# Optimization experiments

Hardware: AMD Instinct MI355X
Metric: run time of the kernel (lower is better)

Reference implementation:

```python
import jax, jax.numpy as jnp
import numpy as np

N, E = 50000, 400000
IN_CH, HID, HEADS, EDGE_DIM = 128, 64, 4, 3
NEG_SLOPE = 0.2


def gatv2_conv(x, src, dst, edge_attr, Wl, Wr, We, att, bias):
    # x: [N, F_in]; Wl/Wr: [H*C, F_in]; We: [H*C, edge_dim]; att: [H, C]; bias: [C]
    H, C = att.shape
    n = x.shape[0]
    xl = (x @ Wl.T).reshape(n, H, C)   # source-side transform (lin_l)
    xr = (x @ Wr.T).reshape(n, H, C)   # target-side transform (lin_r)
    e = (edge_attr @ We.T).reshape(-1, H, C)
    z = jax.nn.leaky_relu(xl[src] + xr[dst] + e, NEG_SLOPE)  # [E,H,C]
    alpha = jnp.einsum('ehc,hc->eh', z, att)                 # [E,H]
    # segment softmax over incoming edges per destination node
    amax = jax.ops.segment_max(alpha, dst, num_segments=n)
    alpha = jnp.exp(alpha - amax[dst])
    denom = jax.ops.segment_sum(alpha, dst, num_segments=n)
    alpha = alpha / (denom[dst] + 1e-16)
    msg = xl[src] * alpha[:, :, None]                        # [E,H,C]
    out = jax.ops.segment_sum(msg, dst, num_segments=n)      # [N,H,C]
    return out.mean(axis=1) + bias                           # concat=False -> head mean


def setup_inputs() -> dict:
    key = jax.random.key(0)
    ks = jax.random.split(key, 16)
    s = 0.1
    return {
        'x': jax.random.normal(ks[0], (N, IN_CH), jnp.float32),
        'edge_index': jax.random.randint(ks[1], (2, E), 0, N, jnp.int32),
        'edge_attr': jax.random.normal(ks[2], (E, EDGE_DIM), jnp.float32),
        'Wl1': jax.random.normal(ks[3], (HEADS * HID, IN_CH), jnp.float32) * s,
        'Wr1': jax.random.normal(ks[4], (HEADS * HID, IN_CH), jnp.float32) * s,
        'We1': jax.random.normal(ks[5], (HEADS * HID, EDGE_DIM), jnp.float32) * s,
        'att1': jax.random.normal(ks[6], (HEADS, HID), jnp.float32) * s,
        'b1': jnp.zeros((HID,), jnp.float32),
        'Wl2': jax.random.normal(ks[7], (HEADS * HID, HID), jnp.float32) * s,
        'Wr2': jax.random.normal(ks[8], (HEADS * HID, HID), jnp.float32) * s,
        'We2': jax.random.normal(ks[9], (HEADS * HID, EDGE_DIM), jnp.float32) * s,
        'att2': jax.random.normal(ks[10], (HEADS, HID), jnp.float32) * s,
        'b2': jnp.zeros((HID,), jnp.float32),
        'prelu_w': jnp.full((HID,), 0.25, jnp.float32),
    }


def reference(x, edge_index, edge_attr, Wl1, Wr1, We1, att1, b1, Wl2, Wr2, We2, att2, b2, prelu_w):
    src, dst = edge_index[0], edge_index[1]
    h = gatv2_conv(x, src, dst, edge_attr, Wl1, Wr1, We1, att1, b1)
    h = gatv2_conv(h, src, dst, edge_attr, Wl2, Wr2, We2, att2, b2)
    return jnp.where(h >= 0, h, prelu_w * h)  # PReLU, per-channel weight
```

## Files before the change

### kernel.cpp

```cpp
#include <hip/hip_runtime.h>
#include <hip/hip_bf16.h>

#define HC 256

typedef __attribute__((ext_vector_type(8))) short bf16x8;
typedef __attribute__((ext_vector_type(4))) float f32x4;
typedef __attribute__((ext_vector_type(2))) float f32x2;

__device__ __forceinline__ void gl_lds16(const void* g, void* l) {
  __builtin_amdgcn_global_load_lds(
      (const __attribute__((address_space(1))) unsigned int*)g,
      (__attribute__((address_space(3))) unsigned int*)l, 16, 0, 0);
}

__device__ __forceinline__ void cast_w_one(const float* Wl, const float* Wr,
                                           ushort* WT, int F, int idx) {
  int col = idx / F, f = idx - col * F;
  float v = (col < 256) ? Wl[col * F + f] : Wr[(col - 256) * F + f];
  __hip_bfloat16 h = __float2bfloat16(v);
  WT[(size_t)col * F + f] = *(ushort*)&h;
}

__global__ void k_weights_hist(const float* __restrict__ Wl1, const float* __restrict__ Wr1,
                               ushort* __restrict__ WT1, const float* __restrict__ Wl2,
                               const float* __restrict__ Wr2, ushort* __restrict__ WT2,
                               const int* __restrict__ ei, int* __restrict__ deg, int E_) {
  int idx = blockIdx.x * blockDim.x + threadIdx.x;
  const int t1 = 512 * 128, t2 = 512 * 64;
  if (idx < t1) {
    cast_w_one(Wl1, Wr1, WT1, 128, idx);
  } else if (idx < t1 + t2) {
    cast_w_one(Wl2, Wr2, WT2, 64, idx - t1);
  } else {
    int e = idx - t1 - t2;
    if (e < E_) atomicAdd(&deg[ei[E_ + e]], 1);
  }
}

template <int F>
__global__ __launch_bounds__(256) void gemm_mfma(const ushort* __restrict__ A,
                                                 const ushort* __restrict__ WT,
                                                 ushort* __restrict__ xlb,
                                                 ushort* __restrict__ xrb, int n_nodes) {
  constexpr int NSTEP = F / 64;
  constexpr int SM = (2 * NSTEP * 8192 > 17408) ? 2 * NSTEP * 8192 : 17408;
  __shared__ __align__(16) ushort smem[SM];
  const int tid = threadIdx.x;
  const int wv = tid >> 6, lane = tid & 63;
  const int m16 = lane & 15, quad = lane >> 4;
  const int col0 = blockIdx.x * 128;
  const int row0 = blockIdx.y * 128;
  const int wm = (wv >> 1) * 64, wn = (wv & 1) * 64;

  f32x4 acc[4][4];
#pragma unroll
  for (int i = 0; i < 4; ++i)
#pragma unroll
    for (int j = 0; j < 4; ++j) acc[i][j] = (f32x4){0.f, 0.f, 0.f, 0.f};

  auto load_step = [&](int s) {
    ushort* As = smem + s * 16384;
    ushort* Bs = As + 8192;
    const int khat = s * 64;
#pragma unroll
    for (int t = 0; t < 4; ++t) {
      const int sl16 = tid + 256 * t;
      const int row = sl16 >> 3, sl = sl16 & 7;
      const int gch = sl ^ (row & 7);
      const int grow = row0 + row;
      if (grow < n_nodes)
        gl_lds16(A + (size_t)grow * F + khat + gch * 8, As + sl16 * 8);
      gl_lds16(WT + (size_t)(col0 + row) * F + khat + gch * 8, Bs + sl16 * 8);
    }
  };

  auto mfma_step = [&](int s) {
    ushort* As = smem + s * 16384;
    ushort* Bs = As + 8192;
#pragma unroll
    for (int kh = 0; kh < 2; ++kh) {
      bf16x8 af[4], bf[4];
#pragma unroll
      for (int i = 0; i < 4; ++i) {
        const int row = wm + i * 16 + m16;
        const int slot = (kh * 4 + quad) ^ (row & 7);
        af[i] = *(bf16x8*)&As[row * 64 + slot * 8];
      }
#pragma unroll
      for (int j = 0; j < 4; ++j) {
        const int col = wn + j * 16 + m16;
        const int slot = (kh * 4 + quad) ^ (col & 7);
        bf[j] = *(bf16x8*)&Bs[col * 64 + slot * 8];
      }
#pragma unroll
      for (int i = 0; i < 4; ++i)
#pragma unroll
        for (int j = 0; j < 4; ++j)
          acc[i][j] =
              __builtin_amdgcn_mfma_f32_16x16x32_bf16(af[i], bf[j], acc[i][j], 0, 0, 0);
    }
  };

  load_step(0);
  __syncthreads();
  if (NSTEP > 1) load_step(1);
  mfma_step(0);
  if (NSTEP > 1) {
    __syncthreads();
    mfma_step(1);
  }

  __syncthreads();
  ushort* Ct = smem;
#pragma unroll
  for (int i = 0; i < 4; ++i) {
#pragma unroll
    for (int r = 0; r < 4; ++r) {
      const int row = wm + i * 16 + quad * 4 + r;
#pragma unroll
      for (int j = 0; j < 4; ++j) {
        __hip_bfloat16 h = __float2bfloat16(acc[i][j][r]);
        Ct[row * 136 + wn + j * 16 + m16] = *(ushort*)&h;
      }
    }
  }
  __syncthreads();
  const bool is_xl = (col0 < 256);
  ushort* dst = is_xl ? xlb : xrb;
  const int cb = is_xl ? col0 : (col0 - 256);
  const int chunk = tid & 15;
#pragma unroll
  for (int it = 0; it < 8; ++it) {
    const int row = (tid >> 4) + 16 * it;
    const int grow = row0 + row;
    int4 v = *(int4*)&Ct[row * 136 + chunk * 8];
    if (grow < n_nodes)
      *(int4*)(dst + (size_t)grow * 256 + cb + chunk * 8) = v;
  }
}

__global__ void k_scan_local(const int* __restrict__ deg, int* __restrict__ rowstart,
                             int* __restrict__ partial, int n) {
  __shared__ int a[256], b[256];
  const int t = threadIdx.x;
  const int i = blockIdx.x * 256 + t;
  const int v = (i < n) ? deg[i] : 0;
  a[t] = v;
  __syncthreads();
  int* cur = a;
  int* nxt = b;
  for (int off = 1; off < 256; off <<= 1) {
    int x = cur[t];
    if (t >= off) x += cur[t - off];
    nxt[t] = x;
    __syncthreads();
    int* tmp = cur; cur = nxt; nxt = tmp;
  }
  const int incl = cur[t];
  if (i < n) rowstart[i] = incl - v;
  if (t == 255) partial[blockIdx.x] = incl;
}

__global__ void k_scan_final(const int* __restrict__ partial, int nblk,
                             int* __restrict__ rowstart, int* __restrict__ cursor,
                             float4* __restrict__ sea, int n, int E_) {
  __shared__ int a[256], b[256];
  const int t = threadIdx.x;
  const int v = (t < nblk) ? partial[t] : 0;
  a[t] = v;
  __syncthreads();
  int* cur = a;
  int* nxt = b;
  for (int off = 1; off < 256; off <<= 1) {
    int x = cur[t];
    if (t >= off) x += cur[t - off];
    nxt[t] = x;
    __syncthreads();
    int* tmp = cur; cur = nxt; nxt = tmp;
  }
  const int boff = (blockIdx.x > 0) ? cur[blockIdx.x - 1] : 0;
  const int i = blockIdx.x * 256 + t;
  if (i < n) {
    int vv = rowstart[i] + boff;
    rowstart[i] = vv;
    cursor[i] = vv;
  }
  if (i == 0) rowstart[n] = E_;
  if (blockIdx.x == 0 && t < 8) sea[E_ + t] = make_float4(0.f, 0.f, 0.f, 0.f);
}

__global__ void k_prep(const float* __restrict__ x, ushort* __restrict__ A,
                       const int* __restrict__ ei, const float* __restrict__ ea,
                       int* __restrict__ cursor, float4* __restrict__ sea,
                       int n, int E_) {
  const int nx8 = n * 16;
  int idx = blockIdx.x * blockDim.x + threadIdx.x;
  if (idx < nx8) {
    const float4* xp = (const float4*)x + (size_t)idx * 2;
    float4 v0 = xp[0], v1 = xp[1];
    float vv[8] = {v0.x, v0.y, v0.z, v0.w, v1.x, v1.y, v1.z, v1.w};
    __align__(16) ushort hb[8];
#pragma unroll
    for (int j = 0; j < 8; ++j) {
      __hip_bfloat16 h = __float2bfloat16(vv[j]);
      hb[j] = *(ushort*)&h;
    }
    *(int4*)(A + (size_t)idx * 8) = *(int4*)hb;
  } else {
    int e = idx - nx8;
    if (e < E_) {
      int dst = ei[E_ + e];
      int pos = atomicAdd(&cursor[dst], 1);
      sea[pos] = make_float4(ea[e * 3], ea[e * 3 + 1], ea[e * 3 + 2],
                             __int_as_float(ei[e]));
    }
  }
}

__device__ __forceinline__ float dpp_ror_add(float p) {
  p += __int_as_float(__builtin_amdgcn_update_dpp(
      0, __float_as_int(p), 0x128, 0xF, 0xF, true));
  p += __int_as_float(__builtin_amdgcn_update_dpp(
      0, __float_as_int(p), 0x124, 0xF, 0xF, true));
  p += __int_as_float(__builtin_amdgcn_update_dpp(
      0, __float_as_int(p), 0x122, 0xF, 0xF, true));
  p += __int_as_float(__builtin_amdgcn_update_dpp(
      0, __float_as_int(p), 0x121, 0xF, 0xF, true));
  return p;
}

__device__ __forceinline__ void edge_step(
    const ushort4& lu, const float4& eav, const f32x2* we0, const f32x2* we1,
    const f32x2* we2, const f32x2* at6, const f32x2* at4, const f32x2* xrl,
    f32x2& num01, f32x2& num23, float& den) {
  f32x2 lav0, lav1;
  lav0.x = __uint_as_float((unsigned)lu.x << 16);
  lav0.y = __uint_as_float((unsigned)lu.y << 16);
  lav1.x = __uint_as_float((unsigned)lu.z << 16);
  lav1.y = __uint_as_float((unsigned)lu.w << 16);
  f32x2 pv = {0.f, 0.f};
#pragma unroll
  for (int j = 0; j < 2; ++j) {
    f32x2 la = (j == 0) ? lav0 : lav1;
    f32x2 t = xrl[j] + we0[j] * eav.x;
    t = t + we1[j] * eav.y;
    t = t + we2[j] * eav.z;
    f32x2 s = t + la;
    f32x2 sa = {fabsf(s.x), fabsf(s.y)};
    pv = pv + at6[j] * s;
    pv = pv + at4[j] * sa;
  }
  float p = pv.x + pv.y;
  p = dpp_ror_add(p);
  const float w = exp2f(p);
  den += w;
  num01 = num01 + (f32x2){w, w} * lav0;
  num23 = num23 + (f32x2){w, w} * lav1;
}

template <int MODE>
__global__ __launch_bounds__(64) void fused_attn(
    const ushort* __restrict__ xlb, const ushort* __restrict__ xrb,
    const int* __restrict__ rowstart, const float4* __restrict__ sea,
    const float* __restrict__ We, const float* __restrict__ att,
    const float* __restrict__ bias, const float* __restrict__ pw,
    float* __restrict__ out, ushort* __restrict__ outs, int n, int chunk) {
  const int lane = threadIdx.x;
  const int d0 = blockIdx.x * chunk;
  if (d0 >= n) return;
  const int d1 = min(d0 + chunk, n);

  f32x2 we0[2], we1[2], we2[2], at6[2], at4[2];
  const float L2E = 1.4426950408889634f;
#pragma unroll
  for (int j = 0; j < 4; ++j) {
    int r = 4 * lane + j;
    ((float*)we0)[j] = We[r * 3 + 0];
    ((float*)we1)[j] = We[r * 3 + 1];
    ((float*)we2)[j] = We[r * 3 + 2];
    float a = att[r];
    ((float*)at6)[j] = a * (0.6f * L2E);
    ((float*)at4)[j] = a * (0.4f * L2E);
  }
  const float4 bias4 = ((const float4*)bias)[lane & 15];
  float4 pw4 = {0.f, 0.f, 0.f, 0.f};
  if (MODE == 1) pw4 = ((const float4*)pw)[lane & 15];
  const ushort4* xlb4 = (const ushort4*)xlb;

  for (int d = d0; d < d1; ++d) {
    const ushort4 xu = ((const ushort4*)xrb)[(unsigned)(d * 64) + lane];
    f32x2 xrl[2];
    xrl[0].x = __uint_as_float((unsigned)xu.x << 16);
    xrl[0].y = __uint_as_float((unsigned)xu.y << 16);
    xrl[1].x = __uint_as_float((unsigned)xu.z << 16);
    xrl[1].y = __uint_as_float((unsigned)xu.w << 16);

    int pos = rowstart[d];
    const int end = rowstart[d + 1];
    f32x2 num01 = {0.f, 0.f}, num23 = {0.f, 0.f};
    float den = 0.f;

    if (pos < end) {
      float4 e0 = sea[pos], e1 = sea[pos + 1], e2 = sea[pos + 2], e3 = sea[pos + 3];
      ushort4 g0 = xlb4[(unsigned)(__float_as_int(e0.w) * 64) + lane];
      ushort4 g1 = xlb4[(unsigned)(__float_as_int(e1.w) * 64) + lane];
      ushort4 g2 = xlb4[(unsigned)(__float_as_int(e2.w) * 64) + lane];
      ushort4 g3 = xlb4[(unsigned)(__float_as_int(e3.w) * 64) + lane];

      while (pos + 4 <= end) {
        ushort4 h0 = g0, h1 = g1, h2 = g2, h3 = g3;
        float4 f0 = e0, f1 = e1, f2 = e2, f3 = e3;
        if (pos + 4 < end) {
          f0 = sea[pos + 4];
          f1 = sea[pos + 5];
          f2 = sea[pos + 6];
          f3 = sea[pos + 7];
          h0 = xlb4[(unsigned)(__float_as_int(f0.w) * 64) + lane];
          h1 = xlb4[(unsigned)(__float_as_int(f1.w) * 64) + lane];
          h2 = xlb4[(unsigned)(__float_as_int(f2.w) * 64) + lane];
          h3 = xlb4[(unsigned)(__float_as_int(f3.w) * 64) + lane];
        }
        edge_step(g0, e0, we0, we1, we2, at6, at4, xrl, num01, num23, den);
        edge_step(g1, e1, we0, we1, we2, at6, at4, xrl, num01, num23, den);
        edge_step(g2, e2, we0, we1, we2, at6, at4, xrl, num01, num23, den);
        edge_step(g3, e3, we0, we1, we2, at6, at4, xrl, num01, num23, den);
        g0 = h0; g1 = h1; g2 = h2; g3 = h3;
        e0 = f0; e1 = f1; e2 = f2; e3 = f3;
        pos += 4;
      }
      const int rem = end - pos;
      if (rem > 0) edge_step(g0, e0, we0, we1, we2, at6, at4, xrl, num01, num23, den);
      if (rem > 1) edge_step(g1, e1, we0, we1, we2, at6, at4, xrl, num01, num23, den);
      if (rem > 2) edge_step(g2, e2, we0, we1, we2, at6, at4, xrl, num01, num23, den);
    }

    const float inv = 1.f / (den + 1e-16f);
    float4 r;
    r.x = num01.x * inv;
    r.y = num01.y * inv;
    r.z = num23.x * inv;
    r.w = num23.y * inv;
    r.x += __shfl_xor(r.x, 16);
    r.y += __shfl_xor(r.y, 16);
    r.z += __shfl_xor(r.z, 16);
    r.w += __shfl_xor(r.w, 16);
    r.x += __shfl_xor(r.x, 32);
    r.y += __shfl_xor(r.y, 32);
    r.z += __shfl_xor(r.z, 32);
    r.w += __shfl_xor(r.w, 32);
    if (lane < 16) {
      float o[4];
      o[0] = 0.25f * r.x + bias4.x;
      o[1] = 0.25f * r.y + bias4.y;
      o[2] = 0.25f * r.z + bias4.z;
      o[3] = 0.25f * r.w + bias4.w;
      if (MODE == 1) {
        const float pwv[4] = {pw4.x, pw4.y, pw4.z, pw4.w};
#pragma unroll
        for (int j = 0; j < 4; ++j) o[j] = (o[j] >= 0.f) ? o[j] : pwv[j] * o[j];
        ((float4*)out)[(size_t)d * 16 + lane] = make_float4(o[0], o[1], o[2], o[3]);
      } else {
        ushort hb[4];
#pragma unroll
        for (int j = 0; j < 4; ++j) {
          __hip_bfloat16 h = __float2bfloat16(o[j]);
          hb[j] = *(ushort*)&h;
        }
        *(ushort4*)(outs + (size_t)d * 64 + 4 * lane) =
            make_ushort4(hb[0], hb[1], hb[2], hb[3]);
      }
    }
  }
}

extern "C" void kernel_launch(void* const* d_in, const int* in_sizes, int n_in,
                              void* d_out, int out_size, void* d_ws, size_t ws_size,
                              hipStream_t stream) {
  const float* x    = (const float*)d_in[0];
  const int*   ei   = (const int*)d_in[1];
  const float* ea   = (const float*)d_in[2];
  const float* Wl1  = (const float*)d_in[3];
  const float* Wr1  = (const float*)d_in[4];
  const float* We1  = (const float*)d_in[5];
  const float* att1 = (const float*)d_in[6];
  const float* b1   = (const float*)d_in[7];
  const float* Wl2  = (const float*)d_in[8];
  const float* Wr2  = (const float*)d_in[9];
  const float* We2  = (const float*)d_in[10];
  const float* att2 = (const float*)d_in[11];
  const float* b2   = (const float*)d_in[12];
  const float* pw   = (const float*)d_in[13];
  const int N_ = in_sizes[0] / 128;
  const int E_ = in_sizes[1] / 2;
  float* out = (float*)d_out;

  char* w = (char*)d_ws;
  auto alloc = [&](size_t bytes) {
    char* p = w;
    w += (bytes + 255) & ~size_t(255);
    return p;
  };
  ushort* xlb      = (ushort*)alloc((size_t)N_ * 256 * 2);
  ushort* xrb      = (ushort*)alloc((size_t)N_ * 256 * 2);
  ushort* Ax       = (ushort*)alloc((size_t)N_ * 128 * 2);
  ushort* h2       = (ushort*)alloc((size_t)N_ * 64 * 2);
  float4* sea      = (float4*)alloc((size_t)(E_ + 8) * 16);
  int*    deg      = (int*)alloc((size_t)N_ * 4);
  int*    rowstart = (int*)alloc((size_t)(N_ + 1) * 4);
  int*    cursor   = (int*)alloc((size_t)N_ * 4);
  int*    partial  = (int*)alloc(256 * 4);
  ushort* WT1      = (ushort*)alloc((size_t)512 * 128 * 2);
  ushort* WT2      = (ushort*)alloc((size_t)512 * 64 * 2);

  hipMemsetAsync(deg, 0, (size_t)N_ * 4, stream);
  const int wtot = 512 * 128 + 512 * 64 + E_;
  k_weights_hist<<<(wtot + 255) / 256, 256, 0, stream>>>(Wl1, Wr1, WT1, Wl2, Wr2, WT2,
                                                         ei, deg, E_);

  const int nblk = (N_ + 255) / 256;
  k_scan_local<<<nblk, 256, 0, stream>>>(deg, rowstart, partial, N_);
  k_scan_final<<<nblk, 256, 0, stream>>>(partial, nblk, rowstart, cursor, sea, N_, E_);
  const int ptot = N_ * 16 + E_;
  k_prep<<<(ptot + 255) / 256, 256, 0, stream>>>(x, Ax, ei, ea, cursor, sea, N_, E_);

  const dim3 GG(4, (N_ + 127) / 128);
  const int chunk = 2;
  const int FB = (N_ + chunk - 1) / chunk;

  gemm_mfma<128><<<GG, 256, 0, stream>>>(Ax, WT1, xlb, xrb, N_);
  fused_attn<0><<<FB, 64, 0, stream>>>(xlb, xrb, rowstart, sea, We1, att1,
                                       b1, pw, nullptr, h2, N_, chunk);
  gemm_mfma<64><<<GG, 256, 0, stream>>>(h2, WT2, xlb, xrb, N_);
  fused_attn<1><<<FB, 64, 0, stream>>>(xlb, xrb, rowstart, sea, We2, att2,
                                       b2, pw, out, nullptr, N_, chunk);
}
```

Baseline: 261.3 us.

## Split wavefront into two half-waves each handling a destination node with 16B gathers

The attention kernel now gives each 32-lane half of the wavefront its own destination node. Each lane handles 8 channels and gathers 16-byte rows instead of 8-byte ones. The head reduction drops to three DPP steps, the leaky-relu dot is folded into one scaled FMA form, and the weight loads are vectorised. This aims to cut per-edge instruction count and raise memory-level parallelism, at the cost of more registers per lane and load imbalance between the two halves when their degrees differ.

Result: slower. 356.1 us (+36.3%).

```diff
diff --git a/kernel.cpp b/kernel.cpp
--- a/kernel.cpp
+++ b/kernel.cpp
@@ -4,6 +4,7 @@
 #define HC 256
 
 typedef __attribute__((ext_vector_type(8))) short bf16x8;
+typedef __attribute__((ext_vector_type(8))) unsigned short u16x8;
 typedef __attribute__((ext_vector_type(4))) float f32x4;
 typedef __attribute__((ext_vector_type(2))) float f32x2;
 
@@ -217,160 +218,178 @@
   }
 }
 
-__device__ __forceinline__ float dpp_ror_add(float p) {
+__device__ __forceinline__ float dpp_add8(float p) {
   p += __int_as_float(__builtin_amdgcn_update_dpp(
-      0, __float_as_int(p), 0x128, 0xF, 0xF, true));
+      0, __float_as_int(p), 0xB1, 0xF, 0xF, true));
   p += __int_as_float(__builtin_amdgcn_update_dpp(
-      0, __float_as_int(p), 0x124, 0xF, 0xF, true));
+      0, __float_as_int(p), 0x4E, 0xF, 0xF, true));
   p += __int_as_float(__builtin_amdgcn_update_dpp(
-      0, __float_as_int(p), 0x122, 0xF, 0xF, true));
-  p += __int_as_float(__builtin_amdgcn_update_dpp(
-      0, __float_as_int(p), 0x121, 0xF, 0xF, true));
+      0, __float_as_int(p), 0x141, 0xF, 0xF, true));
   return p;
 }
 
-__device__ __forceinline__ void edge_step(
-    const ushort4& lu, const float4& eav, const f32x2* we0, const f32x2* we1,
-    const f32x2* we2, const f32x2* at6, const f32x2* at4, const f32x2* xrl,
-    f32x2& num01, f32x2& num23, float& den) {
-  f32x2 lav0, lav1;
-  lav0.x = __uint_as_float((unsigned)lu.x << 16);
-  lav0.y = __uint_as_float((unsigned)lu.y << 16);
-  lav1.x = __uint_as_float((unsigned)lu.z << 16);
-  lav1.y = __uint_as_float((unsigned)lu.w << 16);
+__device__ __forceinline__ void expand8(const u16x8& v, f32x2* o) {
+#pragma unroll
+  for (int t = 0; t < 4; ++t) {
+    o[t].x = __uint_as_float((unsigned)v[2 * t] << 16);
+    o[t].y = __uint_as_float((unsigned)v[2 * t + 1] << 16);
+  }
+}
+
+__device__ __forceinline__ void edge_step2(
+    const u16x8& lu, const float4& eav, const f32x2* we0, const f32x2* we1,
+    const f32x2* we2, const f32x2* at6, const f32x2* xrl,
+    f32x2* num, float& den) {
+  f32x2 la[4];
+  expand8(lu, la);
   f32x2 pv = {0.f, 0.f};
 #pragma unroll
-  for (int j = 0; j < 2; ++j) {
-    f32x2 la = (j == 0) ? lav0 : lav1;
+  for (int j = 0; j < 4; ++j) {
     f32x2 t = xrl[j] + we0[j] * eav.x;
     t = t + we1[j] * eav.y;
     t = t + we2[j] * eav.z;
-    f32x2 s = t + la;
-    f32x2 sa = {fabsf(s.x), fabsf(s.y)};
-    pv = pv + at6[j] * s;
-    pv = pv + at4[j] * sa;
+    f32x2 s = t + la[j];
+    f32x2 u;
+    u.x = fmaf(fabsf(s.x), 0.66666667f, s.x);
+    u.y = fmaf(fabsf(s.y), 0.66666667f, s.y);
+    pv = pv + at6[j] * u;
   }
   float p = pv.x + pv.y;
-  p = dpp_ror_add(p);
+  p = dpp_add8(p);
   const float w = exp2f(p);
   den += w;
-  num01 = num01 + (f32x2){w, w} * lav0;
-  num23 = num23 + (f32x2){w, w} * lav1;
+#pragma unroll
+  for (int j = 0; j < 4; ++j) num[j] = num[j] + (f32x2){w, w} * la[j];
 }
 
 template <int MODE>
-__global__ __launch_bounds__(64) void fused_attn(
+__global__ __launch_bounds__(64, 4) void fused_attn(
     const ushort* __restrict__ xlb, const ushort* __restrict__ xrb,
     const int* __restrict__ rowstart, const float4* __restrict__ sea,
     const float* __restrict__ We, const float* __restrict__ att,
     const float* __restrict__ bias, const float* __restrict__ pw,
-    float* __restrict__ out, ushort* __restrict__ outs, int n, int chunk) {
+    float* __restrict__ out, ushort* __restrict__ outs, int n, int chp) {
   const int lane = threadIdx.x;
-  const int d0 = blockIdx.x * chunk;
+  const int half = lane >> 5;
+  const int hl = lane & 31;
+  const int d0 = blockIdx.x * (2 * chp);
   if (d0 >= n) return;
-  const int d1 = min(d0 + chunk, n);
-
-  f32x2 we0[2], we1[2], we2[2], at6[2], at4[2];
-  const float L2E = 1.4426950408889634f;
-#pragma unroll
-  for (int j = 0; j < 4; ++j) {
-    int r = 4 * lane + j;
-    ((float*)we0)[j] = We[r * 3 + 0];
-    ((float*)we1)[j] = We[r * 3 + 1];
-    ((float*)we2)[j] = We[r * 3 + 2];
-    float a = att[r];
-    ((float*)at6)[j] = a * (0.6f * L2E);
-    ((float*)at4)[j] = a * (0.4f * L2E);
-  }
-  const float4 bias4 = ((const float4*)bias)[lane & 15];
-  float4 pw4 = {0.f, 0.f, 0.f, 0.f};
-  if (MODE == 1) pw4 = ((const float4*)pw)[lane & 15];
-  const ushort4* xlb4 = (const ushort4*)xlb;
-
-  for (int d = d0; d < d1; ++d) {
-    const ushort4 xu = ((const ushort4*)xrb)[(unsigned)(d * 64) + lane];
-    f32x2 xrl[2];
-    xrl[0].x = __uint_as_float((unsigned)xu.x << 16);
-    xrl[0].y = __uint_as_float((unsigned)xu.y << 16);
-    xrl[1].x = __uint_as_float((unsigned)xu.z << 16);
-    xrl[1].y = __uint_as_float((unsigned)xu.w << 16);
-
-    int pos = rowstart[d];
-    const int end = rowstart[d + 1];
-    f32x2 num01 = {0.f, 0.f}, num23 = {0.f, 0.f};
+
+  float wf[24];
+  {
+    const float4* Wq = (const float4*)We + 6 * hl;
+#pragma unroll
+    for (int t = 0; t < 6; ++t) *(float4*)&wf[4 * t] = Wq[t];
+  }
+  float af[8];
+  {
+    const float4* Aq = (const float4*)att + 2 * hl;
+    *(float4*)&af[0] = Aq[0];
+    *(float4*)&af[4] = Aq[1];
+  }
+  f32x2 we0[4], we1[4], we2[4], at6[4];
+  const float C6 = 0.6f * 1.4426950408889634f;
+#pragma unroll
+  for (int j = 0; j < 8; ++j) {
+    ((float*)we0)[j] = wf[3 * j + 0];
+    ((float*)we1)[j] = wf[3 * j + 1];
+    ((float*)we2)[j] = wf[3 * j + 2];
+    ((float*)at6)[j] = af[j] * C6;
+  }
+  const int cb8 = 8 * (hl & 7);
+  const float4 biasA = *(const float4*)&bias[cb8];
+  const float4 biasB = *(const float4*)&bias[cb8 + 4];
+  float4 pwA = {0.f, 0.f, 0.f, 0.f}, pwB = {0.f, 0.f, 0.f, 0.f};
+  if (MODE == 1) {
+    pwA = *(const float4*)&pw[cb8];
+    pwB = *(const float4*)&pw[cb8 + 4];
+  }
+
+#define GAT(e_) (*(const u16x8*)&xlb[(size_t)(unsigned)__float_as_int((e_).w) * 256 + hl * 8])
+
+  for (int k = 0; k < chp; ++k) {
+    const int dd = d0 + 2 * k + half;
+    const bool dv = dd < n;
+    const int dc = dv ? dd : n - 1;
+
+    u16x8 xu = *(const u16x8*)&xrb[(size_t)dc * 256 + hl * 8];
+    f32x2 xrl[4];
+    expand8(xu, xrl);
+
+    int pos = rowstart[dc];
+    const int end = dv ? rowstart[dc + 1] : pos;
+    f32x2 num[4] = {{0.f, 0.f}, {0.f, 0.f}, {0.f, 0.f}, {0.f, 0.f}};
     float den = 0.f;
 
     if (pos < end) {
       float4 e0 = sea[pos], e1 = sea[pos + 1], e2 = sea[pos + 2], e3 = sea[pos + 3];
-      ushort4 g0 = xlb4[(unsigned)(__float_as_int(e0.w) * 64) + lane];
-      ushort4 g1 = xlb4[(unsigned)(__float_as_int(e1.w) * 64) + lane];
-      ushort4 g2 = xlb4[(unsigned)(__float_as_int(e2.w) * 64) + lane];
-      ushort4 g3 = xlb4[(unsigned)(__float_as_int(e3.w) * 64) + lane];
+      u16x8 g0 = GAT(e0), g1 = GAT(e1), g2 = GAT(e2), g3 = GAT(e3);
 
       while (pos + 4 <= end) {
-        ushort4 h0 = g0, h1 = g1, h2 = g2, h3 = g3;
+        u16x8 h0 = g0, h1 = g1, h2 = g2, h3 = g3;
         float4 f0 = e0, f1 = e1, f2 = e2, f3 = e3;
         if (pos + 4 < end) {
           f0 = sea[pos + 4];
           f1 = sea[pos + 5];
           f2 = sea[pos + 6];
           f3 = sea[pos + 7];
-          h0 = xlb4[(unsigned)(__float_as_int(f0.w) * 64) + lane];
-          h1 = xlb4[(unsigned)(__float_as_int(f1.w) * 64) + lane];
-          h2 = xlb4[(unsigned)(__float_as_int(f2.w) * 64) + lane];
-          h3 = xlb4[(unsigned)(__float_as_int(f3.w) * 64) + lane];
+          h0 = GAT(f0); h1 = GAT(f1); h2 = GAT(f2); h3 = GAT(f3);
         }
-        edge_step(g0, e0, we0, we1, we2, at6, at4, xrl, num01, num23, den);
-        edge_step(g1, e1, we0, we1, we2, at6, at4, xrl, num01, num23, den);
-        edge_step(g2, e2, we0, we1, we2, at6, at4, xrl, num01, num23, den);
-        edge_step(g3, e3, we0, we1, we2, at6, at4, xrl, num01, num23, den);
+        edge_step2(g0, e0, we0, we1, we2, at6, xrl, num, den);
+        edge_step2(g1, e1, we0, we1, we2, at6, xrl, num, den);
+        edge_step2(g2, e2, we0, we1, we2, at6, xrl, num, den);
+        edge_step2(g3, e3, we0, we1, we2, at6, xrl, num, den);
         g0 = h0; g1 = h1; g2 = h2; g3 = h3;
         e0 = f0; e1 = f1; e2 = f2; e3 = f3;
         pos += 4;
       }
       const int rem = end - pos;
-      if (rem > 0) edge_step(g0, e0, we0, we1, we2, at6, at4, xrl, num01, num23, den);
-      if (rem > 1) edge_step(g1, e1, we0, we1, we2, at6, at4, xrl, num01, num23, den);
-      if (rem > 2) edge_step(g2, e2, we0, we1, we2, at6, at4, xrl, num01, num23, den);
+      if (rem > 0) edge_step2(g0, e0, we0, we1, we2, at6, xrl, num, den);
+      if (rem > 1) edge_step2(g1, e1, we0, we1, we2, at6, xrl, num, den);
+      if (rem > 2) edge_step2(g2, e2, we0, we1, we2, at6, xrl, num, den);
     }
 
     const float inv = 1.f / (den + 1e-16f);
-    float4 r;
-    r.x = num01.x * inv;
-    r.y = num01.y * inv;
-    r.z = num23.x * inv;
-    r.w = num23.y * inv;
-    r.x += __shfl_xor(r.x, 16);
-    r.y += __shfl_xor(r.y, 16);
-    r.z += __shfl_xor(r.z, 16);
-    r.w += __shfl_xor(r.w, 16);
-    r.x += __shfl_xor(r.x, 32);
-    r.y += __shfl_xor(r.y, 32);
-    r.z += __shfl_xor(r.z, 32);
-    r.w += __shfl_xor(r.w, 32);
-    if (lane < 16) {
-      float o[4];
-      o[0] = 0.25f * r.x + bias4.x;
-      o[1] = 0.25f * r.y + bias4.y;
-      o[2] = 0.25f * r.z + bias4.z;
-      o[3] = 0.25f * r.w + bias4.w;
+    float rr[8];
+#pragma unroll
+    for (int t = 0; t < 4; ++t) {
+      rr[2 * t] = num[t].x * inv;
+      rr[2 * t + 1] = num[t].y * inv;
+    }
+#pragma unroll
+    for (int t = 0; t < 8; ++t) {
+      rr[t] += __shfl_xor(rr[t], 8);
+      rr[t] += __shfl_xor(rr[t], 16);
+    }
+    if (hl < 8 && dv) {
+      float o[8];
+      o[0] = 0.25f * rr[0] + biasA.x;
+      o[1] = 0.25f * rr[1] + biasA.y;
+      o[2] = 0.25f * rr[2] + biasA.z;
+      o[3] = 0.25f * rr[3] + biasA.w;
+      o[4] = 0.25f * rr[4] + biasB.x;
+      o[5] = 0.25f * rr[5] + biasB.y;
+      o[6] = 0.25f * rr[6] + biasB.z;
+      o[7] = 0.25f * rr[7] + biasB.w;
       if (MODE == 1) {
-        const float pwv[4] = {pw4.x, pw4.y, pw4.z, pw4.w};
-#pragma unroll
-        for (int j = 0; j < 4; ++j) o[j] = (o[j] >= 0.f) ? o[j] : pwv[j] * o[j];
-        ((float4*)out)[(size_t)d * 16 + lane] = make_float4(o[0], o[1], o[2], o[3]);
+        const float pwv[8] = {pwA.x, pwA.y, pwA.z, pwA.w, pwB.x, pwB.y, pwB.z, pwB.w};
+#pragma unroll
+        for (int j = 0; j < 8; ++j) o[j] = (o[j] >= 0.f) ? o[j] : pwv[j] * o[j];
+        float* op = out + (size_t)dd * 64 + hl * 8;
+        *(float4*)op = make_float4(o[0], o[1], o[2], o[3]);
+        *(float4*)(op + 4) = make_float4(o[4], o[5], o[6], o[7]);
       } else {
-        ushort hb[4];
-#pragma unroll
-        for (int j = 0; j < 4; ++j) {
+        u16x8 hb;
+#pragma unroll
+        for (int j = 0; j < 8; ++j) {
           __hip_bfloat16 h = __float2bfloat16(o[j]);
           hb[j] = *(ushort*)&h;
         }
-        *(ushort4*)(outs + (size_t)d * 64 + 4 * lane) =
-            make_ushort4(hb[0], hb[1], hb[2], hb[3]);
+        *(u16x8*)(outs + (size_t)dd * 64 + hl * 8) = hb;
       }
     }
   }
+#undef GAT
 }
 
 extern "C" void kernel_launch(void* const* d_in, const int* in_sizes, int n_in,
@@ -424,13 +443,13 @@
   k_prep<<<(ptot + 255) / 256, 256, 0, stream>>>(x, Ax, ei, ea, cursor, sea, N_, E_);
 
   const dim3 GG(4, (N_ + 127) / 128);
-  const int chunk = 2;
-  const int FB = (N_ + chunk - 1) / chunk;
+  const int chp = 2;
+  const int FB = (N_ + 2 * chp - 1) / (2 * chp);
 
   gemm_mfma<128><<<GG, 256, 0, stream>>>(Ax, WT1, xlb, xrb, N_);
   fused_attn<0><<<FB, 64, 0, stream>>>(xlb, xrb, rowstart, sea, We1, att1,
-                                       b1, pw, nullptr, h2, N_, chunk);
+                                       b1, pw, nullptr, h2, N_, chp);
   gemm_mfma<64><<<GG, 256, 0, stream>>>(h2, WT2, xlb, xrb, N_);
   fused_attn<1><<<FB, 64, 0, stream>>>(xlb, xrb, rowstart, sea, We2, att2,
-                                       b2, pw, out, nullptr, N_, chunk);
-}
+                                       b2, pw, out, nullptr, N_, chp);
+}
```
